# Optimization experiments

Hardware: AMD Instinct MI355X
Metric: run time of the kernel (lower is better)

Reference implementation:

```python
import jax, jax.numpy as jnp
import numpy as np

NX, NY = 512, 512
DX, DY = 1e-4, 1e-4
VS = 1550.0
DT = 2.5e-8


def setup_inputs() -> dict:
    key = jax.random.key(0)
    k1, k2 = jax.random.split(key)
    sensor_data = jax.random.normal(k1, (4, 2, 128, 2048), dtype=jnp.float32)
    sensor_xy = jax.random.randint(k2, (128, 2), 0, 512, dtype=jnp.int32)
    return {"sensor_data": sensor_data, "sensor_xy": sensor_xy}


def _delay_indices(sensor_xy):
    # pixel grids, 1-indexed as in the torch code (arange(1,513))
    ix = jnp.arange(1, NX + 1, dtype=jnp.float32)[None, :, None]  # (1,Nx,1)
    iy = jnp.arange(1, NY + 1, dtype=jnp.float32)[None, None, :]  # (1,1,Ny)
    x = sensor_xy[:, 0].astype(jnp.float32)[:, None, None]        # (S,1,1)
    y = sensor_xy[:, 1].astype(jnp.float32)[:, None, None]
    dis = jnp.sqrt(((x - ix + 1.0) * DX) ** 2 + ((y - iy + 1.0) * DY) ** 2)  # (S,Nx,Ny)
    # .to(torch.long) truncates; values are non-negative so int cast matches
    return (dis / VS / DT).astype(jnp.int32).reshape(sensor_xy.shape[0], -1)  # (S, Nx*Ny)


def reference(sensor_data, sensor_xy):
    B = sensor_data.shape[0]
    S = sensor_xy.shape[0]
    t = _delay_indices(sensor_xy)                           # (S, P) int32
    data = jnp.transpose(sensor_data, (2, 0, 1, 3))         # (S, B, 2, T)

    def step(img, xs):
        t_s, d_s = xs                                       # (P,), (B,2,T)
        return img + d_s[:, :, t_s], None                   # gather + accumulate

    img0 = jnp.zeros((B, 2, NX * NY), dtype=sensor_data.dtype)
    img, _ = jax.lax.scan(step, img0, (t, data))
    return img.reshape(B, 2, NX, NY)
```

## Files before the change

### kernel.cpp

```cpp
#include <hip/hip_runtime.h>
#include <math.h>


#define NXY 512
#define S_CNT 128
#define T_CNT 2048
#define CH 8
#define CH_STRIDE (S_CNT * T_CNT)
#define NPIX (NXY * NXY)
#define TAB_BYTES (NPIX * 2)
#define CHUNK 32
#define NCHUNK (S_CNT / CHUNK)
#define WIN 64
#define PATW 24

#pragma float_control(push)
#pragma float_control(precise, on)
__device__ __forceinline__ unsigned short delay_entry(int adx, int ady) {
    const double DX32 = (double)1e-4f;
    const double R1 = (double)(float)(1.0 / 1550.0);
    const double R2 = (double)(float)(1.0 / (double)2.5e-8f);
    float dxf = (float)((double)adx * DX32);
    float dyf = (float)((double)ady * DX32);
    float a2 = (float)((double)dxf * (double)dxf);
    float b2 = (float)((double)dyf * (double)dyf);
    float sum = (float)((double)a2 + (double)b2);
    float dis = (float)sqrt((double)sum);
    float q1 = (float)((double)dis * R1);
    float q2 = (float)((double)q1 * R2);
    return (unsigned short)(int)q2;
}

__device__ __forceinline__ unsigned int bf16_rne(float f) {
    unsigned int x = __float_as_uint(f);
    return (x + 0x7fffu + ((x >> 16) & 1u)) >> 16;
}

__global__ __launch_bounds__(256) void prep(const float* __restrict__ data,
                                            unsigned short* __restrict__ tab,
                                            uint4* __restrict__ d2b) {
    int idx = blockIdx.x * 256 + threadIdx.x;
    tab[idx] = delay_entry(idx >> 9, idx & 511);

    unsigned int w[4];
#pragma unroll
    for (int j = 0; j < 4; ++j) {
        unsigned int lo = bf16_rne(data[(2 * j) * CH_STRIDE + idx]);
        unsigned int hi = bf16_rne(data[(2 * j + 1) * CH_STRIDE + idx]);
        w[j] = lo | (hi << 16);
    }
    d2b[idx] = make_uint4(w[0], w[1], w[2], w[3]);
}

__device__ __forceinline__ int tmin_entry(int adx, int ady) {
    return (int)delay_entry(adx, ady);
}
#pragma float_control(pop)

__device__ __forceinline__ float bflo(unsigned int u) { return __uint_as_float(u << 16); }
__device__ __forceinline__ float bfhi(unsigned int u) { return __uint_as_float(u & 0xffff0000u); }

__global__ __launch_bounds__(256) void das_gather_lds(const uint4* __restrict__ d2b,
                                                      const unsigned short* __restrict__ tab,
                                                      const int* __restrict__ sxy,
                                                      float* __restrict__ out) {
    __shared__ int4 meta[S_CNT];
    __shared__ uint4 winb[CHUNK * WIN];
    __shared__ uint4 patb[CHUNK * 16 * 3];
    const unsigned short* pat16 = (const unsigned short*)patb;

    int tid = threadIdx.x;
    int x0 = (blockIdx.x >> 5) << 4;
    int y0 = (blockIdx.x & 31) << 4;

    if (tid < S_CNT) {
        int sxv = sxy[2 * tid];
        int syv = sxy[2 * tid + 1];
        int axm = sxv < x0 ? x0 - sxv : (sxv > x0 + 15 ? sxv - x0 - 15 : 0);
        int aym = syv < y0 ? y0 - syv : (syv > y0 + 15 ? syv - y0 - 15 : 0);
        int ay0 = aym & ~7;
        int tmin = tmin_entry(axm, aym);
        meta[tid] = make_int4(sxv, syv, axm | (ay0 << 16), tmin);
    }
    __syncthreads();

    int iy = y0 | (((tid >> 6) & 1) << 3) | (tid & 7);
    int ix = x0 | ((tid >> 7) << 3) | ((tid >> 3) & 7);

    float acc[CH];
#pragma unroll
    for (int k = 0; k < CH; ++k) acc[k] = 0.0f;

    for (int c = 0; c < NCHUNK; ++c) {
        int s0 = c * CHUNK;

        {
            int lsw = tid >> 3;
            int tm = meta[s0 + lsw].w;
            const uint4* src = d2b + ((s0 + lsw) << 11) + tm;
            int e0 = tid & 7;
#pragma unroll
            for (int j = 0; j < 8; ++j)
                winb[(lsw << 6) + e0 + 8 * j] = src[e0 + 8 * j];
        }

#pragma unroll
        for (int j = 0; j < 6; ++j) {
            unsigned int idx = (unsigned int)tid + 256u * j;
            unsigned int r3 = idx / 3u;
            unsigned int cc = idx - r3 * 3u;
            unsigned int row = r3 & 15u;
            unsigned int ls = r3 >> 4;
            int4 m = meta[s0 + ls];
            int ax0 = m.z & 0xffff;
            int ay0 = m.z >> 16;
            const uint4* src = (const uint4*)((const char*)tab +
                (((size_t)(ax0 + (int)row) << 10) + ((size_t)ay0 << 1) + ((size_t)cc << 4)));
            patb[ls * 48u + row * 3u + cc] = *src;
        }
        __syncthreads();

#pragma unroll 4
        for (int ls = 0; ls < CHUNK; ++ls) {
            int4 m = meta[s0 + ls];
            int dxi = m.x - ix;
            int dyi = m.y - iy;
            int adx = dxi < 0 ? -dxi : dxi;
            int ady = dyi < 0 ? -dyi : dyi;
            int ax0 = m.z & 0xffff;
            int ay0 = m.z >> 16;
            int t = (int)pat16[ls * (16 * PATW) + (adx - ax0) * PATW + (ady - ay0)];
            uint4 w = winb[(ls << 6) + (t - m.w)];
            acc[0] += bflo(w.x);
            acc[1] += bfhi(w.x);
            acc[2] += bflo(w.y);
            acc[3] += bfhi(w.y);
            acc[4] += bflo(w.z);
            acc[5] += bfhi(w.z);
            acc[6] += bflo(w.w);
            acc[7] += bfhi(w.w);
        }
        __syncthreads();
    }

    int pix = (ix << 9) | iy;
#pragma unroll
    for (int k = 0; k < CH; ++k) out[k * NPIX + pix] = acc[k];
}

#pragma float_control(push)
#pragma float_control(precise, on)
__global__ __launch_bounds__(256) void build_table(unsigned short* __restrict__ tab) {
    int idx = blockIdx.x * 256 + threadIdx.x;
    tab[idx] = delay_entry(idx >> 9, idx & 511);
}
#pragma float_control(pop)

__global__ __launch_bounds__(256) void das_main(const float* __restrict__ data,
                                                const unsigned short* __restrict__ tab,
                                                const int* __restrict__ sxy,
                                                float* __restrict__ out) {
    __shared__ int sx[S_CNT];
    __shared__ int sy[S_CNT];
    int tid = threadIdx.x;
    if (tid < S_CNT) {
        sx[tid] = sxy[2 * tid];
        sy[tid] = sxy[2 * tid + 1];
    }
    __syncthreads();
    int iy = ((blockIdx.x & 31) << 4) | (tid & 15);
    int ix = ((blockIdx.x >> 5) << 4) | (tid >> 4);
    float acc[CH];
#pragma unroll
    for (int k = 0; k < CH; ++k) acc[k] = 0.0f;
#pragma unroll 4
    for (int s = 0; s < S_CNT; ++s) {
        int dxi = sx[s] - ix;
        int dyi = sy[s] - iy;
        int adx = dxi < 0 ? -dxi : dxi;
        int ady = dyi < 0 ? -dyi : dyi;
        int t = (int)tab[(adx << 9) | ady];
        const float* p = data + (s << 11) + t;
#pragma unroll
        for (int k = 0; k < CH; ++k) acc[k] += p[(size_t)k * CH_STRIDE];
    }
    int pix = (ix << 9) | iy;
#pragma unroll
    for (int k = 0; k < CH; ++k) out[k * NPIX + pix] = acc[k];
}

extern "C" void kernel_launch(void* const* d_in, const int* in_sizes, int n_in,
                              void* d_out, int out_size, void* d_ws, size_t ws_size,
                              hipStream_t stream) {
    const float* data = (const float*)d_in[0];
    const int* sxy = (const int*)d_in[1];
    float* out = (float*)d_out;
    unsigned short* tab = (unsigned short*)d_ws;

    size_t need = (size_t)TAB_BYTES + (size_t)CH_STRIDE * 16;
    if (ws_size >= need) {
        uint4* d2b = (uint4*)((char*)d_ws + TAB_BYTES);
        prep<<<NPIX / 256, 256, 0, stream>>>(data, tab, d2b);
        das_gather_lds<<<1024, 256, 0, stream>>>(d2b, tab, sxy, out);
    } else {
        build_table<<<NPIX / 256, 256, 0, stream>>>(tab);
        das_main<<<1024, 256, 0, stream>>>(data, tab, sxy, out);
    }
}
```

Before: 106.0 us.

## Vectorize prep kernel and split gather into index pass plus accumulate pass

The prep kernel now handles four elements per thread, using float4 loads and wider table stores. The gather kernel subtracts each sensor's tmin from the pattern-table entries while staging them, and packs per-sensor metadata into smaller uint2 records with precomputed offsets. The per-chunk inner loop becomes two fully unrolled passes. The first computes all 32 window indices into registers, and the second does the LDS loads and accumulation, giving more independent loads in flight. The 32-entry index array raises register pressure, which may reduce occupancy.

New measurement: 117.1 us. 1.1x slower.

```diff
diff --git a/kernel.cpp b/kernel.cpp
--- a/kernel.cpp
+++ b/kernel.cpp
@@ -13,6 +13,7 @@
 #define NCHUNK (S_CNT / CHUNK)
 #define WIN 64
 #define PATW 24
+#define PAT_STRIDE (16 * PATW)
 
 #pragma float_control(push)
 #pragma float_control(precise, on)
@@ -36,20 +37,34 @@
     return (x + 0x7fffu + ((x >> 16) & 1u)) >> 16;
 }
 
-__global__ __launch_bounds__(256) void prep(const float* __restrict__ data,
-                                            unsigned short* __restrict__ tab,
-                                            uint4* __restrict__ d2b) {
-    int idx = blockIdx.x * 256 + threadIdx.x;
-    tab[idx] = delay_entry(idx >> 9, idx & 511);
-
-    unsigned int w[4];
-#pragma unroll
-    for (int j = 0; j < 4; ++j) {
-        unsigned int lo = bf16_rne(data[(2 * j) * CH_STRIDE + idx]);
-        unsigned int hi = bf16_rne(data[(2 * j + 1) * CH_STRIDE + idx]);
-        w[j] = lo | (hi << 16);
-    }
-    d2b[idx] = make_uint4(w[0], w[1], w[2], w[3]);
+__global__ __launch_bounds__(256) void prep4(const float* __restrict__ data,
+                                             unsigned short* __restrict__ tab,
+                                             uint4* __restrict__ d2b) {
+    int g = blockIdx.x * 256 + threadIdx.x;
+    unsigned int t01, t23;
+    {
+        int i0 = 4 * g;
+        t01 = (unsigned int)delay_entry(i0 >> 9, i0 & 511) |
+              ((unsigned int)delay_entry((i0 + 1) >> 9, (i0 + 1) & 511) << 16);
+        t23 = (unsigned int)delay_entry((i0 + 2) >> 9, (i0 + 2) & 511) |
+              ((unsigned int)delay_entry((i0 + 3) >> 9, (i0 + 3) & 511) << 16);
+    }
+    ((uint2*)tab)[g] = make_uint2(t01, t23);
+
+    const float4* data4 = (const float4*)data;
+    float4 v[CH];
+#pragma unroll
+    for (int ch = 0; ch < CH; ++ch) v[ch] = data4[ch * (CH_STRIDE / 4) + g];
+#pragma unroll
+    for (int q = 0; q < 4; ++q) {
+        const float* e0 = (const float*)&v[0];
+        unsigned int w0 = bf16_rne(((const float*)&v[0])[q]) | (bf16_rne(((const float*)&v[1])[q]) << 16);
+        unsigned int w1 = bf16_rne(((const float*)&v[2])[q]) | (bf16_rne(((const float*)&v[3])[q]) << 16);
+        unsigned int w2 = bf16_rne(((const float*)&v[4])[q]) | (bf16_rne(((const float*)&v[5])[q]) << 16);
+        unsigned int w3 = bf16_rne(((const float*)&v[6])[q]) | (bf16_rne(((const float*)&v[7])[q]) << 16);
+        d2b[4 * g + q] = make_uint4(w0, w1, w2, w3);
+        (void)e0;
+    }
 }
 
 __device__ __forceinline__ int tmin_entry(int adx, int ady) {
@@ -60,11 +75,18 @@
 __device__ __forceinline__ float bflo(unsigned int u) { return __uint_as_float(u << 16); }
 __device__ __forceinline__ float bfhi(unsigned int u) { return __uint_as_float(u & 0xffff0000u); }
 
-__global__ __launch_bounds__(256) void das_gather_lds(const uint4* __restrict__ d2b,
+__device__ __forceinline__ unsigned int sub16x2(unsigned int a, unsigned int t) {
+    unsigned int lo = (a - t) & 0xffffu;
+    unsigned int hi = ((a >> 16) - t) << 16;
+    return lo | hi;
+}
+
+__global__ __launch_bounds__(256) void das_gather_ilp(const uint4* __restrict__ d2b,
                                                       const unsigned short* __restrict__ tab,
                                                       const int* __restrict__ sxy,
                                                       float* __restrict__ out) {
-    __shared__ int4 meta[S_CNT];
+    __shared__ uint2 minfo[S_CNT];
+    __shared__ uint2 mstage[S_CNT];
     __shared__ uint4 winb[CHUNK * WIN];
     __shared__ uint4 patb[CHUNK * 16 * 3];
     const unsigned short* pat16 = (const unsigned short*)patb;
@@ -80,7 +102,9 @@
         int aym = syv < y0 ? y0 - syv : (syv > y0 + 15 ? syv - y0 - 15 : 0);
         int ay0 = aym & ~7;
         int tmin = tmin_entry(axm, aym);
-        meta[tid] = make_int4(sxv, syv, axm | (ay0 << 16), tmin);
+        minfo[tid] = make_uint2((unsigned int)(sxv | (syv << 16)),
+                                (unsigned int)(axm * PATW + ay0));
+        mstage[tid] = make_uint2((unsigned int)(axm | (ay0 << 16)), (unsigned int)tmin);
     }
     __syncthreads();
 
@@ -96,7 +120,7 @@
 
         {
             int lsw = tid >> 3;
-            int tm = meta[s0 + lsw].w;
+            int tm = (int)mstage[s0 + lsw].y;
             const uint4* src = d2b + ((s0 + lsw) << 11) + tm;
             int e0 = tid & 7;
 #pragma unroll
@@ -111,26 +135,38 @@
             unsigned int cc = idx - r3 * 3u;
             unsigned int row = r3 & 15u;
             unsigned int ls = r3 >> 4;
-            int4 m = meta[s0 + ls];
-            int ax0 = m.z & 0xffff;
-            int ay0 = m.z >> 16;
+            uint2 st = mstage[s0 + ls];
+            int ax0 = (int)(st.x & 0xffffu);
+            int ay0 = (int)(st.x >> 16);
+            unsigned int tm = st.y;
             const uint4* src = (const uint4*)((const char*)tab +
                 (((size_t)(ax0 + (int)row) << 10) + ((size_t)ay0 << 1) + ((size_t)cc << 4)));
-            patb[ls * 48u + row * 3u + cc] = *src;
+            uint4 v = *src;
+            v.x = sub16x2(v.x, tm);
+            v.y = sub16x2(v.y, tm);
+            v.z = sub16x2(v.z, tm);
+            v.w = sub16x2(v.w, tm);
+            patb[ls * 48u + row * 3u + cc] = v;
         }
         __syncthreads();
 
-#pragma unroll 4
+        unsigned int tw[CHUNK];
+#pragma unroll
         for (int ls = 0; ls < CHUNK; ++ls) {
-            int4 m = meta[s0 + ls];
-            int dxi = m.x - ix;
-            int dyi = m.y - iy;
+            uint2 mi = minfo[s0 + ls];
+            int sxv = (int)(mi.x & 0xffffu);
+            int syv = (int)(mi.x >> 16);
+            int dxi = sxv - ix;
+            int dyi = syv - iy;
             int adx = dxi < 0 ? -dxi : dxi;
             int ady = dyi < 0 ? -dyi : dyi;
-            int ax0 = m.z & 0xffff;
-            int ay0 = m.z >> 16;
-            int t = (int)pat16[ls * (16 * PATW) + (adx - ax0) * PATW + (ady - ay0)];
-            uint4 w = winb[(ls << 6) + (t - m.w)];
+            int pidx = adx * PATW + ady - (int)mi.y;
+            tw[ls] = (unsigned int)pat16[ls * PAT_STRIDE + pidx];
+        }
+
+#pragma unroll
+        for (int ls = 0; ls < CHUNK; ++ls) {
+            uint4 w = winb[(ls << 6) + tw[ls]];
             acc[0] += bflo(w.x);
             acc[1] += bfhi(w.x);
             acc[2] += bflo(w.y);
@@ -200,8 +236,8 @@
     size_t need = (size_t)TAB_BYTES + (size_t)CH_STRIDE * 16;
     if (ws_size >= need) {
         uint4* d2b = (uint4*)((char*)d_ws + TAB_BYTES);
-        prep<<<NPIX / 256, 256, 0, stream>>>(data, tab, d2b);
-        das_gather_lds<<<1024, 256, 0, stream>>>(d2b, tab, sxy, out);
+        prep4<<<NPIX / 1024, 256, 0, stream>>>(data, tab, d2b);
+        das_gather_ilp<<<1024, 256, 0, stream>>>(d2b, tab, sxy, out);
     } else {
         build_table<<<NPIX / 256, 256, 0, stream>>>(tab);
         das_main<<<1024, 256, 0, stream>>>(data, tab, sxy, out);
```

## Gather bf16 samples directly from global memory with SAD-based index math

Applied to the files above, without the earlier changes.

Removes the per-chunk LDS window staging of sensor samples and instead gathers each pixel's 16-byte bf16 sample vector straight from global memory (L2-cached) using a pre-scaled byte offset. The delay table now stores delays pre-shifted by 4 so they serve directly as byte offsets. Pattern lookups use v_sad_u32 to fold abs-difference and offset into one instruction, and accumulation uses packed float2 adds. This trades LDS traffic and a sync-heavy copy for scattered global/L2 gathers, with the risk of higher latency per load. Pre-shifting into 16 bits also limits delays to below 4096.

New measurement: 111.6 us. 5.3% more time.

```diff
diff --git a/kernel.cpp b/kernel.cpp
--- a/kernel.cpp
+++ b/kernel.cpp
@@ -11,8 +11,21 @@
 #define TAB_BYTES (NPIX * 2)
 #define CHUNK 32
 #define NCHUNK (S_CNT / CHUNK)
-#define WIN 64
 #define PATW 24
+#define PAT_ROW_B (PATW * 2)
+#define PAT_SENS_B (16 * PAT_ROW_B)
+
+typedef float f32x2 __attribute__((ext_vector_type(2)));
+
+#if __has_builtin(__builtin_amdgcn_sad_u32)
+__device__ __forceinline__ unsigned int sadu(unsigned int a, unsigned int b, unsigned int c) {
+    return __builtin_amdgcn_sad_u32(a, b, c);
+}
+#else
+__device__ __forceinline__ unsigned int sadu(unsigned int a, unsigned int b, unsigned int c) {
+    return (a > b ? a - b : b - a) + c;
+}
+#endif
 
 #pragma float_control(push)
 #pragma float_control(precise, on)
@@ -40,7 +53,7 @@
                                             unsigned short* __restrict__ tab,
                                             uint4* __restrict__ d2b) {
     int idx = blockIdx.x * 256 + threadIdx.x;
-    tab[idx] = delay_entry(idx >> 9, idx & 511);
+    tab[idx] = (unsigned short)((unsigned int)delay_entry(idx >> 9, idx & 511) << 4);
 
     unsigned int w[4];
 #pragma unroll
@@ -51,23 +64,18 @@
     }
     d2b[idx] = make_uint4(w[0], w[1], w[2], w[3]);
 }
-
-__device__ __forceinline__ int tmin_entry(int adx, int ady) {
-    return (int)delay_entry(adx, ady);
-}
 #pragma float_control(pop)
 
 __device__ __forceinline__ float bflo(unsigned int u) { return __uint_as_float(u << 16); }
 __device__ __forceinline__ float bfhi(unsigned int u) { return __uint_as_float(u & 0xffff0000u); }
 
-__global__ __launch_bounds__(256) void das_gather_lds(const uint4* __restrict__ d2b,
-                                                      const unsigned short* __restrict__ tab,
-                                                      const int* __restrict__ sxy,
-                                                      float* __restrict__ out) {
-    __shared__ int4 meta[S_CNT];
-    __shared__ uint4 winb[CHUNK * WIN];
+__global__ __launch_bounds__(256) void das_sad(const uint4* __restrict__ d2b,
+                                               const unsigned short* __restrict__ tab,
+                                               const int* __restrict__ sxy,
+                                               float* __restrict__ out) {
+    __shared__ uint4 minfo[S_CNT];
+    __shared__ unsigned int mstage[S_CNT];
     __shared__ uint4 patb[CHUNK * 16 * 3];
-    const unsigned short* pat16 = (const unsigned short*)patb;
 
     int tid = threadIdx.x;
     int x0 = (blockIdx.x >> 5) << 4;
@@ -79,30 +87,25 @@
         int axm = sxv < x0 ? x0 - sxv : (sxv > x0 + 15 ? sxv - x0 - 15 : 0);
         int aym = syv < y0 ? y0 - syv : (syv > y0 + 15 ? syv - y0 - 15 : 0);
         int ay0 = aym & ~7;
-        int tmin = tmin_entry(axm, aym);
-        meta[tid] = make_int4(sxv, syv, axm | (ay0 << 16), tmin);
+        minfo[tid] = make_uint4((unsigned int)sxv, (unsigned int)(2 * syv),
+                                (unsigned int)(-(axm * 48 + ay0 * 2)), 0u);
+        mstage[tid] = (unsigned int)(axm | (ay0 << 16));
     }
     __syncthreads();
 
     int iy = y0 | (((tid >> 6) & 1) << 3) | (tid & 7);
     int ix = x0 | ((tid >> 7) << 3) | ((tid >> 3) & 7);
-
-    float acc[CH];
-#pragma unroll
-    for (int k = 0; k < CH; ++k) acc[k] = 0.0f;
+    unsigned int uix = (unsigned int)ix;
+    unsigned int uiy2 = (unsigned int)(2 * iy);
+
+    f32x2 acc2[4];
+#pragma unroll
+    for (int k = 0; k < 4; ++k) acc2[k] = (f32x2){0.0f, 0.0f};
+
+    const char* patc = (const char*)patb;
 
     for (int c = 0; c < NCHUNK; ++c) {
         int s0 = c * CHUNK;
-
-        {
-            int lsw = tid >> 3;
-            int tm = meta[s0 + lsw].w;
-            const uint4* src = d2b + ((s0 + lsw) << 11) + tm;
-            int e0 = tid & 7;
-#pragma unroll
-            for (int j = 0; j < 8; ++j)
-                winb[(lsw << 6) + e0 + 8 * j] = src[e0 + 8 * j];
-        }
 
 #pragma unroll
         for (int j = 0; j < 6; ++j) {
@@ -111,41 +114,43 @@
             unsigned int cc = idx - r3 * 3u;
             unsigned int row = r3 & 15u;
             unsigned int ls = r3 >> 4;
-            int4 m = meta[s0 + ls];
-            int ax0 = m.z & 0xffff;
-            int ay0 = m.z >> 16;
+            unsigned int st = mstage[s0 + ls];
+            int ax0 = (int)(st & 0xffffu);
+            int ay0 = (int)(st >> 16);
             const uint4* src = (const uint4*)((const char*)tab +
                 (((size_t)(ax0 + (int)row) << 10) + ((size_t)ay0 << 1) + ((size_t)cc << 4)));
             patb[ls * 48u + row * 3u + cc] = *src;
         }
         __syncthreads();
 
-#pragma unroll 4
+        const char* d2bc = (const char*)d2b + ((size_t)s0 << 15);
+#pragma unroll 8
         for (int ls = 0; ls < CHUNK; ++ls) {
-            int4 m = meta[s0 + ls];
-            int dxi = m.x - ix;
-            int dyi = m.y - iy;
-            int adx = dxi < 0 ? -dxi : dxi;
-            int ady = dyi < 0 ? -dyi : dyi;
-            int ax0 = m.z & 0xffff;
-            int ay0 = m.z >> 16;
-            int t = (int)pat16[ls * (16 * PATW) + (adx - ax0) * PATW + (ady - ay0)];
-            uint4 w = winb[(ls << 6) + (t - m.w)];
-            acc[0] += bflo(w.x);
-            acc[1] += bfhi(w.x);
-            acc[2] += bflo(w.y);
-            acc[3] += bfhi(w.y);
-            acc[4] += bflo(w.z);
-            acc[5] += bfhi(w.z);
-            acc[6] += bflo(w.w);
-            acc[7] += bfhi(w.w);
+            uint4 mi = minfo[s0 + ls];
+            unsigned int b1 = sadu(mi.x, uix, 0u);
+            unsigned int b2 = sadu(mi.y, uiy2, mi.z);
+            unsigned int byte = b1 * 48u + b2;
+            unsigned int t16 = (unsigned int)*(const unsigned short*)(
+                patc + (size_t)(ls * PAT_SENS_B) + byte);
+            uint4 w = *(const uint4*)(d2bc + ((size_t)ls << 15) + t16);
+            f32x2 p0 = {bflo(w.x), bfhi(w.x)};
+            f32x2 p1 = {bflo(w.y), bfhi(w.y)};
+            f32x2 p2 = {bflo(w.z), bfhi(w.z)};
+            f32x2 p3 = {bflo(w.w), bfhi(w.w)};
+            acc2[0] += p0;
+            acc2[1] += p1;
+            acc2[2] += p2;
+            acc2[3] += p3;
         }
         __syncthreads();
     }
 
     int pix = (ix << 9) | iy;
 #pragma unroll
-    for (int k = 0; k < CH; ++k) out[k * NPIX + pix] = acc[k];
+    for (int k = 0; k < 4; ++k) {
+        out[(2 * k) * NPIX + pix] = acc2[k].x;
+        out[(2 * k + 1) * NPIX + pix] = acc2[k].y;
+    }
 }
 
 #pragma float_control(push)
@@ -201,7 +206,7 @@
     if (ws_size >= need) {
         uint4* d2b = (uint4*)((char*)d_ws + TAB_BYTES);
         prep<<<NPIX / 256, 256, 0, stream>>>(data, tab, d2b);
-        das_gather_lds<<<1024, 256, 0, stream>>>(d2b, tab, sxy, out);
+        das_sad<<<1024, 256, 0, stream>>>(d2b, tab, sxy, out);
     } else {
         build_table<<<NPIX / 256, 256, 0, stream>>>(tab);
         das_main<<<1024, 256, 0, stream>>>(data, tab, sxy, out);
```
